# Kernel tuning notes

Hardware: AMD Instinct MI355X
Metric: run time of the kernel (lower is better)

Reference implementation:

```python
import jax, jax.numpy as jnp
import numpy as np

EMBED_DIM = 1024
NUM_HEADS = 16
HEAD_DIM = EMBED_DIM // NUM_HEADS
EPS = 1e-5


def setup_inputs() -> dict:
    key = jax.random.key(0)
    ks = jax.random.split(key, 14)
    B, S, E = 2, 2048, EMBED_DIM
    s = 1.0 / np.sqrt(E)
    inp = {
        "x": jax.random.normal(ks[0], (B, S, E), dtype=jnp.float32),
        "Wq": jax.random.normal(ks[1], (E, E), dtype=jnp.float32) * s,
        "bq": jax.random.normal(ks[2], (E,), dtype=jnp.float32) * 0.01,
        "Wk": jax.random.normal(ks[3], (E, E), dtype=jnp.float32) * s,
        "bk": jax.random.normal(ks[4], (E,), dtype=jnp.float32) * 0.01,
        "Wv": jax.random.normal(ks[5], (E, E), dtype=jnp.float32) * s,
        "bv": jax.random.normal(ks[6], (E,), dtype=jnp.float32) * 0.01,
        "Wo": jax.random.normal(ks[7], (E, E), dtype=jnp.float32) * s,
        "bo": jax.random.normal(ks[8], (E,), dtype=jnp.float32) * 0.01,
        "qn_w": jnp.ones((HEAD_DIM,), jnp.float32) + 0.1 * jax.random.normal(ks[9], (HEAD_DIM,), jnp.float32),
        "qn_b": 0.1 * jax.random.normal(ks[10], (HEAD_DIM,), jnp.float32),
        "kn_w": jnp.ones((HEAD_DIM,), jnp.float32) + 0.1 * jax.random.normal(ks[11], (HEAD_DIM,), jnp.float32),
        "kn_b": 0.1 * jax.random.normal(ks[12], (HEAD_DIM,), jnp.float32),
    }
    return inp


def _layernorm(t, w, b):
    # normalize over last axis (head_dim), matching eqx.nn.LayerNorm(eps=1e-5)
    mu = jnp.mean(t, axis=-1, keepdims=True)
    var = jnp.mean(jnp.square(t - mu), axis=-1, keepdims=True)
    return (t - mu) * jax.lax.rsqrt(var + EPS) * w + b


def reference(x, Wq, bq, Wk, bk, Wv, bv, Wo, bo, qn_w, qn_b, kn_w, kn_b):
    B, S, E = x.shape
    H, D = NUM_HEADS, HEAD_DIM
    q = (x @ Wq.T + bq).reshape(B, S, H, D)
    k = (x @ Wk.T + bk).reshape(B, S, H, D)
    v = (x @ Wv.T + bv).reshape(B, S, H, D)
    q = _layernorm(q, qn_w, qn_b)
    k = _layernorm(k, kn_w, kn_b)
    scale = D ** (-0.5)
    # [B,H,S,S] score matrix (faithful to naive implementation)
    scores = jnp.einsum("bqhd,bkhd->bhqk", q, k) * scale
    attn = jax.nn.softmax(scores, axis=-1)
    out = jnp.einsum("bhqk,bkhd->bqhd", attn, v).reshape(B, S, E)
    return out @ Wo.T + bo
```

## Files before the change

### kernel.cpp

```cpp
#include <hip/hip_runtime.h>
#include <stdint.h>


typedef __bf16 bf16_t;
typedef __bf16 bf16x8 __attribute__((ext_vector_type(8)));
typedef __bf16 bf16x4 __attribute__((ext_vector_type(4)));
typedef __bf16 bf16x2 __attribute__((ext_vector_type(2)));
typedef float f32x4 __attribute__((ext_vector_type(4)));
typedef float f32x16 __attribute__((ext_vector_type(16)));
typedef uint32_t u32x4 __attribute__((ext_vector_type(4)));

#define S_LEN 2048
#define QSCALE 0.1803368801f

__device__ __forceinline__ void load_lds16(const void* g, void* l) {
  __builtin_amdgcn_global_load_lds((__attribute__((address_space(1))) void*)g,
                                   (__attribute__((address_space(3))) void*)l,
                                   16, 0, 0);
}

__device__ __forceinline__ f32x4 mfma16(bf16x8 a, bf16x8 b, f32x4 c) {
  return __builtin_amdgcn_mfma_f32_16x16x32_bf16(a, b, c, 0, 0, 0);
}

__device__ __forceinline__ f32x16 mfma32(bf16x8 a, bf16x8 b, f32x16 c) {
  return __builtin_amdgcn_mfma_f32_32x32x16_bf16(a, b, c, 0, 0, 0);
}

__device__ __forceinline__ uint32_t pk_bf16(float a, float b) {
  bf16x2 v; v[0] = (bf16_t)a; v[1] = (bf16_t)b;
  return __builtin_bit_cast(uint32_t, v);
}

__device__ __forceinline__ void plswap(uint32_t& a, uint32_t& b) {
  asm volatile("v_permlane32_swap_b32 %0, %1" : "+v"(a), "+v"(b));
}

__global__ void cvt_all(const float* __restrict__ x, const float* __restrict__ Wq,
                        const float* __restrict__ Wk, const float* __restrict__ Wv,
                        const float* __restrict__ Wo,
                        bf16_t* __restrict__ xb, bf16_t* __restrict__ Wb,
                        bf16_t* __restrict__ Wob) {
  const int bid = blockIdx.x;
  const float* src; bf16_t* dst; int idx;
  if (bid < 4096) { src = x; dst = xb; idx = bid; }
  else {
    const int r = bid - 4096, rg = r >> 10;
    idx = r & 1023;
    if (rg == 0)      { src = Wq; dst = Wb; }
    else if (rg == 1) { src = Wk; dst = Wb + (1 << 20); }
    else if (rg == 2) { src = Wv; dst = Wb + (2 << 20); }
    else              { src = Wo; dst = Wob; }
  }
  const int i = (idx * 256 + threadIdx.x) * 4;
  float4 v = *reinterpret_cast<const float4*>(src + i);
  bf16x4 o;
  o[0] = (bf16_t)v.x; o[1] = (bf16_t)v.y; o[2] = (bf16_t)v.z; o[3] = (bf16_t)v.w;
  *reinterpret_cast<bf16x4*>(dst + i) = o;
}

__device__ __forceinline__ void gemm_main(const bf16_t* __restrict__ ga,
                                          const bf16_t* __restrict__ gb,
                                          bf16_t* As, bf16_t* Bs,
                                          int t, int wr, int wc, int lg, int lr,
                                          f32x4 (&acc)[4][4]) {
  for (int k0 = 0; k0 < 1024; k0 += 32) {
    load_lds16(ga + k0,          As + t * 8);
    load_lds16(ga + 65536 + k0,  As + 2048 + t * 8);
    load_lds16(gb + k0,          Bs + t * 8);
    load_lds16(gb + 65536 + k0,  Bs + 2048 + t * 8);
    __syncthreads();
    bf16x8 af[4], bfr[4];
#pragma unroll
    for (int mt = 0; mt < 4; ++mt)
      af[mt] = *reinterpret_cast<const bf16x8*>(As + ((wr * 64 + mt * 16 + lr) << 5) + lg * 8);
#pragma unroll
    for (int nt = 0; nt < 4; ++nt)
      bfr[nt] = *reinterpret_cast<const bf16x8*>(Bs + ((wc * 64 + nt * 16 + lr) << 5) + lg * 8);
#pragma unroll
    for (int mt = 0; mt < 4; ++mt)
#pragma unroll
      for (int nt = 0; nt < 4; ++nt)
        acc[mt][nt] = mfma16(af[mt], bfr[nt], acc[mt][nt]);
    __syncthreads();
  }
}

__launch_bounds__(256, 2)
__global__ void gemm_qkv_ln(const bf16_t* __restrict__ A, const bf16_t* __restrict__ Bt,
                            const float* __restrict__ bq, const float* __restrict__ bk,
                            const float* __restrict__ bv,
                            const float* __restrict__ qnw, const float* __restrict__ qnb,
                            const float* __restrict__ knw, const float* __restrict__ knb,
                            bf16_t* __restrict__ Qb, bf16_t* __restrict__ Kb,
                            bf16_t* __restrict__ Vt) {
  __shared__ alignas(16) bf16_t As[128 * 32];
  __shared__ alignas(16) bf16_t Bs[128 * 32];
  const int t = threadIdx.x;
  const int orig = blockIdx.y * 24 + blockIdx.x;
  const int logical = (orig & 7) * 96 + (orig >> 3);
  const int bn = logical % 24, bm = logical / 24;
  const int w = t >> 6, lane = t & 63;
  const int wr = w >> 1, wc = w & 1;
  const int lg = lane >> 4, lr = lane & 15;

  f32x4 acc[4][4] = {};
  const int srow = t >> 2;
  const int scol = (t & 3) << 3;
  const bf16_t* ga = A + ((size_t)(bm * 128 + srow) << 10) + scol;
  const bf16_t* gb = Bt + ((size_t)(bn * 128 + srow) << 10) + scol;
  gemm_main(ga, gb, As, Bs, t, wr, wc, lg, lr, acc);

  const int nbase = bn * 128 + wc * 64;
  const int region = nbase >> 10;
  const int h = (nbase & 1023) >> 6;

  if (region == 2) {
#pragma unroll
    for (int mt = 0; mt < 4; ++mt)
#pragma unroll
      for (int r = 0; r < 4; ++r) {
        const int gm = bm * 128 + wr * 64 + mt * 16 + lg * 4 + r;
        const int b = gm >> 11, s = gm & 2047;
#pragma unroll
        for (int nt = 0; nt < 4; ++nt) {
          const int d = nt * 16 + lr;
          float val = acc[mt][nt][r] + bv[h * 64 + d];
          Vt[((size_t)((b * 16 + h) * 64 + d) << 11) + s] = (bf16_t)val;
        }
      }
  } else {
    const float* bias = region ? bk : bq;
    const float* lw = region ? knw : qnw;
    const float* lb = region ? knb : qnb;
    const float osc = region ? 1.0f : QSCALE;
    bf16_t* Outp = region ? Kb : Qb;
#pragma unroll
    for (int mt = 0; mt < 4; ++mt)
#pragma unroll
      for (int r = 0; r < 4; ++r) {
        const int gm = bm * 128 + wr * 64 + mt * 16 + lg * 4 + r;
        const int b = gm >> 11, s = gm & 2047;
        float vv[4], sum = 0.f, sumsq = 0.f;
#pragma unroll
        for (int nt = 0; nt < 4; ++nt) {
          const int d = nt * 16 + lr;
          vv[nt] = acc[mt][nt][r] + bias[h * 64 + d];
          sum += vv[nt];
          sumsq += vv[nt] * vv[nt];
        }
#pragma unroll
        for (int mk = 1; mk < 16; mk <<= 1) {
          sum += __shfl_xor(sum, mk);
          sumsq += __shfl_xor(sumsq, mk);
        }
        const float mean = sum * (1.f / 64.f);
        const float var = sumsq * (1.f / 64.f) - mean * mean;
        const float rstd = rsqrtf(var + 1e-5f);
        const size_t rowoff = ((size_t)((b * 16 + h) * 2048 + s)) << 6;
#pragma unroll
        for (int nt = 0; nt < 4; ++nt) {
          const int d = nt * 16 + lr;
          float y = ((vv[nt] - mean) * rstd * lw[d] + lb[d]) * osc;
          Outp[rowoff + d] = (bf16_t)y;
        }
      }
  }
}

__launch_bounds__(256, 2)
__global__ void gemm_out(const bf16_t* __restrict__ A, const bf16_t* __restrict__ Bt,
                         const float* __restrict__ bo, float* __restrict__ dout) {
  __shared__ alignas(16) bf16_t As[64 * 32];
  __shared__ alignas(16) bf16_t Bs[128 * 32];
  const int t = threadIdx.x;
  const int orig = blockIdx.y * 8 + blockIdx.x;
  const int logical = (orig & 7) * 64 + (orig >> 3);
  const int bn = logical & 7, bm = logical >> 3;
  const int w = t >> 6, lane = t & 63;
  const int wr = w >> 1, wc = w & 1;
  const int lg = lane >> 4, lr = lane & 15;

  f32x4 acc[2][4] = {};
  const int srow = t >> 2;
  const int scol = (t & 3) << 3;
  const bf16_t* ga = A + ((size_t)(bm * 64 + srow) << 10) + scol;
  const bf16_t* gb = Bt + ((size_t)(bn * 128 + srow) << 10) + scol;

  for (int k0 = 0; k0 < 1024; k0 += 32) {
    load_lds16(ga + k0,          As + t * 8);
    load_lds16(gb + k0,          Bs + t * 8);
    load_lds16(gb + 65536 + k0,  Bs + 2048 + t * 8);
    __syncthreads();
    bf16x8 af[2], bfr[4];
#pragma unroll
    for (int mt = 0; mt < 2; ++mt)
      af[mt] = *reinterpret_cast<const bf16x8*>(As + ((wr * 32 + mt * 16 + lr) << 5) + lg * 8);
#pragma unroll
    for (int nt = 0; nt < 4; ++nt)
      bfr[nt] = *reinterpret_cast<const bf16x8*>(Bs + ((wc * 64 + nt * 16 + lr) << 5) + lg * 8);
#pragma unroll
    for (int mt = 0; mt < 2; ++mt)
#pragma unroll
      for (int nt = 0; nt < 4; ++nt)
        acc[mt][nt] = mfma16(af[mt], bfr[nt], acc[mt][nt]);
    __syncthreads();
  }

#pragma unroll
  for (int mt = 0; mt < 2; ++mt)
#pragma unroll
    for (int r = 0; r < 4; ++r) {
      const int gm = bm * 64 + wr * 32 + mt * 16 + lg * 4 + r;
#pragma unroll
      for (int nt = 0; nt < 4; ++nt) {
        const int gn = bn * 128 + wc * 64 + nt * 16 + lr;
        dout[((size_t)gm << 10) + gn] = acc[mt][nt][r] + bo[gn];
      }
    }
}

template <int NSPLIT>
__launch_bounds__(256, 4)
__global__ void attn_kernel(const bf16_t* __restrict__ Qb, const bf16_t* __restrict__ Kb,
                            const bf16_t* __restrict__ Vt, bf16_t* __restrict__ Og,
                            float* __restrict__ Op, float* __restrict__ Lp) {
  __shared__ alignas(16) bf16_t KVs[4][64 * 64];

  const int t = threadIdx.x;
  const int w = t >> 6, lane = t & 63;
  const int lq = lane & 31;
  const int hi = lane >> 5;
  const int orig = (blockIdx.z * 32 + blockIdx.y) * 16 + blockIdx.x;
  const int logical = (orig & 7) * (64 * NSPLIT) + (orig >> 3);
  const int qt = logical & 15;
  const int bh = (logical >> 4) & 31;
  const int z = (NSPLIT == 1) ? 0 : (logical >> 9);
  const int b = bh >> 4, h = bh & 15;
  const int q0 = qt * 128 + w * 32;
  const int ntiles = 32 / NSPLIT;

  bf16x8 qf[4];
  {
    const bf16_t* qp = Qb + (((size_t)bh * S_LEN + q0 + lq) << 6) + hi * 8;
#pragma unroll
    for (int c = 0; c < 4; ++c)
      qf[c] = *reinterpret_cast<const bf16x8*>(qp + c * 16);
  }

  f32x16 oacc0 = {}, oacc1 = {}, lacc = {};

  const int krow = (t >> 1) & 63;
  const int kch = ((t >> 7) << 1) | (t & 1);
  const bf16_t* kbase = Kb + (((size_t)bh * S_LEN) << 6) + krow * 64 + kch * 8;
  const bf16_t* vbase = Vt + ((size_t)bh << 17) + krow * S_LEN + kch * 8;

#define STAGE(buf, jt)                                                       \
  {                                                                          \
    const bf16_t* kb_ = kbase + (((size_t)(jt)) << 12);                      \
    const bf16_t* vb_ = vbase + (jt) * 64;                                   \
    load_lds16(kb_,      &KVs[buf][t * 8]);                                  \
    load_lds16(kb_ + 32, &KVs[buf][2048 + t * 8]);                           \
    load_lds16(vb_,      &KVs[2 + (buf)][t * 8]);                            \
    load_lds16(vb_ + 32, &KVs[2 + (buf)][2048 + t * 8]);                     \
  }

  STAGE(0, z * ntiles);
  __syncthreads();

  for (int j = 0; j < ntiles; ++j) {
    const int cur = j & 1;
    if (j < ntiles - 1) STAGE(cur ^ 1, z * ntiles + j + 1);

    f32x16 s0 = {}, s1 = {};
    const bf16_t* kr = &KVs[cur][lq * 16 + hi * 8];
#pragma unroll
    for (int c = 0; c < 4; ++c) {
      bf16x8 kf = *reinterpret_cast<const bf16x8*>(kr + c * 1024);
      s0 = mfma32(kf, qf[c], s0);
    }
#pragma unroll
    for (int c = 0; c < 4; ++c) {
      bf16x8 kf = *reinterpret_cast<const bf16x8*>(kr + 512 + c * 1024);
      s1 = mfma32(kf, qf[c], s1);
    }

    f32x16 p0, p1;
#pragma unroll
    for (int i = 0; i < 16; ++i) p0[i] = __builtin_amdgcn_exp2f(s0[i]);
#pragma unroll
    for (int i = 0; i < 16; ++i) p1[i] = __builtin_amdgcn_exp2f(s1[i]);
    lacc += p0;
    lacc += p1;

    const bf16_t* vr = &KVs[2 + cur][lq * 16 + hi * 8];
#pragma unroll
    for (int c = 0; c < 4; ++c) {
      const f32x16 ph = (c < 2) ? p0 : p1;
      const int cl = c & 1;
      uint32_t w00 = pk_bf16(ph[8 * cl + 0], ph[8 * cl + 1]);
      uint32_t w01 = pk_bf16(ph[8 * cl + 2], ph[8 * cl + 3]);
      uint32_t w10 = pk_bf16(ph[8 * cl + 4], ph[8 * cl + 5]);
      uint32_t w11 = pk_bf16(ph[8 * cl + 6], ph[8 * cl + 7]);
      plswap(w00, w10);
      plswap(w01, w11);
      u32x4 pw = {w00, w01, w10, w11};
      bf16x8 pf = __builtin_bit_cast(bf16x8, pw);
      {
        bf16x8 vf = *reinterpret_cast<const bf16x8*>(vr + c * 1024);
        oacc0 = mfma32(vf, pf, oacc0);
      }
      {
        bf16x8 vf = *reinterpret_cast<const bf16x8*>(vr + 512 + c * 1024);
        oacc1 = mfma32(vf, pf, oacc1);
      }
    }
    __syncthreads();
  }

  float l_;
  {
    float sv[8];
#pragma unroll
    for (int i = 0; i < 8; ++i) sv[i] = lacc[i] + lacc[i + 8];
#pragma unroll
    for (int s2 = 4; s2 >= 1; s2 >>= 1)
#pragma unroll
      for (int i = 0; i < s2; ++i) sv[i] += sv[i + s2];
    l_ = sv[0] + __shfl_xor(sv[0], 32);
  }

  if constexpr (NSPLIT == 1) {
    bf16_t* Os = &KVs[0][0] + w * 2048;
    const float inv = __builtin_amdgcn_rcpf(l_);
#pragma unroll
    for (int dh = 0; dh < 2; ++dh) {
      const f32x16 oa = dh ? oacc1 : oacc0;
#pragma unroll
      for (int g = 0; g < 8; ++g) {
        const int reg = g * 2;
        const int dl = (reg & 3) + 8 * (reg >> 2) + 4 * hi;
        const int d = dh * 32 + dl;
        const uint32_t wv = pk_bf16(oa[reg] * inv, oa[reg + 1] * inv);
        const int byte = lq * 128 + ((((d >> 3) ^ (lq & 7))) << 4) + ((d & 7) << 1);
        *reinterpret_cast<uint32_t*>(reinterpret_cast<char*>(Os) + byte) = wv;
      }
    }
#pragma unroll
    for (int it = 0; it < 4; ++it) {
      const int q = it * 8 + (lane >> 3);
      const int ch = lane & 7;
      bf16x8 ov = *reinterpret_cast<const bf16x8*>(
          reinterpret_cast<char*>(Os) + q * 128 + ((ch ^ (q & 7)) << 4));
      const size_t gaddr = (((size_t)(b * S_LEN + q0 + q)) << 10) + h * 64 + ch * 8;
      *reinterpret_cast<bf16x8*>(Og + gaddr) = ov;
    }
  } else {
    float* Os32 = reinterpret_cast<float*>(&KVs[0][0]) + w * 2048;
#pragma unroll
    for (int dh = 0; dh < 2; ++dh) {
      const f32x16 oa = dh ? oacc1 : oacc0;
#pragma unroll
      for (int reg = 0; reg < 16; ++reg) {
        const int dl = (reg & 3) + 8 * (reg >> 2) + 4 * hi;
        const int d = dh * 32 + dl;
        Os32[lq * 64 + (((d >> 2) ^ (lq & 15)) << 2) + (d & 3)] = oa[reg];
      }
    }
    if (lane < 32) Lp[(size_t)(z * 32 + bh) * 2048 + q0 + lq] = l_;
#pragma unroll
    for (int it = 0; it < 4; ++it) {
      const int q = it * 8 + (lane >> 3);
      const size_t rowoff = ((size_t)((z * 32 + bh) * 2048 + q0 + q)) << 6;
#pragma unroll
      for (int c2 = 0; c2 < 2; ++c2) {
        const int ch = ((lane & 7) << 1) + c2;
        f32x4 v = *reinterpret_cast<const f32x4*>(Os32 + q * 64 + ((ch ^ (q & 15)) << 2));
        *reinterpret_cast<f32x4*>(Op + rowoff + (ch << 2)) = v;
      }
    }
  }
#undef STAGE
}

__global__ void attn_combine(const float* __restrict__ Op, const float* __restrict__ Lp,
                             bf16_t* __restrict__ Ob) {
  const int gid = blockIdx.x * 256 + threadIdx.x;
  const int row = gid >> 4, ch = gid & 15;
  const float* o1 = Op + ((size_t)row << 6) + ch * 4;
  const float* o2 = o1 + (1u << 22);
  const float inv = 1.f / (Lp[row] + Lp[(1u << 16) + row]);
  f32x4 v1 = *reinterpret_cast<const f32x4*>(o1);
  f32x4 v2 = *reinterpret_cast<const f32x4*>(o2);
  bf16x4 o;
#pragma unroll
  for (int i = 0; i < 4; ++i) o[i] = (bf16_t)((v1[i] + v2[i]) * inv);
  const int bh = row >> 11, s = row & 2047;
  const int b = bh >> 4, h = bh & 15;
  *reinterpret_cast<bf16x4*>(Ob + (((size_t)(b * S_LEN + s)) << 10) + h * 64 + ch * 4) = o;
}

extern "C" void kernel_launch(void* const* d_in, const int* in_sizes, int n_in,
                              void* d_out, int out_size, void* d_ws, size_t ws_size,
                              hipStream_t stream) {
  const float* x = (const float*)d_in[0];
  const float* Wq = (const float*)d_in[1];
  const float* bq = (const float*)d_in[2];
  const float* Wk = (const float*)d_in[3];
  const float* bk = (const float*)d_in[4];
  const float* Wv = (const float*)d_in[5];
  const float* bv = (const float*)d_in[6];
  const float* Wo = (const float*)d_in[7];
  const float* bo = (const float*)d_in[8];
  const float* qnw = (const float*)d_in[9];
  const float* qnb = (const float*)d_in[10];
  const float* knw = (const float*)d_in[11];
  const float* knb = (const float*)d_in[12];
  float* out = (float*)d_out;

  uint8_t* ws = (uint8_t*)d_ws;
  bf16_t* xb = (bf16_t*)(ws + 0);
  bf16_t* Wb = (bf16_t*)(ws + 8388608);
  bf16_t* Wob = (bf16_t*)(ws + 14680064);
  bf16_t* Qb = (bf16_t*)(ws + 16777216);
  bf16_t* Kb = (bf16_t*)(ws + 25165824);
  bf16_t* Vt = (bf16_t*)(ws + 33554432);
  bf16_t* Ob = (bf16_t*)(ws + 41943040);
  float*  Opart = (float*)(ws + 50331648);
  float*  Lpart = (float*)(ws + 83886080);
  const bool split = ws_size >= 84934656ull;

  cvt_all<<<8192, 256, 0, stream>>>(x, Wq, Wk, Wv, Wo, xb, Wb, Wob);

  gemm_qkv_ln<<<dim3(24, 32), 256, 0, stream>>>(xb, Wb, bq, bk, bv, qnw, qnb, knw, knb,
                                                Qb, Kb, Vt);
  if (split) {
    attn_kernel<2><<<dim3(16, 32, 2), 256, 0, stream>>>(Qb, Kb, Vt, Ob, Opart, Lpart);
    attn_combine<<<4096, 256, 0, stream>>>(Opart, Lpart, Ob);
  } else {
    attn_kernel<1><<<dim3(16, 32, 1), 256, 0, stream>>>(Qb, Kb, Vt, Ob, Opart, Lpart);
  }
  gemm_out<<<dim3(8, 64), 256, 0, stream>>>(Ob, Wob, bo, out);
}
```

Baseline: 122.3 us.

## Double-buffer GEMM LDS tiles and store split-attention partials in bf16

Both GEMM kernels now use two LDS buffers so that the global-to-LDS loads for the next K slice are issued before the MFMAs on the current slice, with one barrier per iteration. This targets load latency that the old load-sync-compute-sync loop exposed. The split-K attention path now writes unnormalized partial outputs in bf16 through the same swizzled LDS staging as the non-split path, and the combine kernel reads them as bf16. This halves partial-buffer traffic at some cost in precision for the unnormalized accumulators, and doubles LDS use in the GEMMs, which could affect occupancy.

After: 117.7 us. -3.7%, faster.

```diff
diff --git a/kernel.cpp b/kernel.cpp
--- a/kernel.cpp
+++ b/kernel.cpp
@@ -59,33 +59,6 @@
   *reinterpret_cast<bf16x4*>(dst + i) = o;
 }
 
-__device__ __forceinline__ void gemm_main(const bf16_t* __restrict__ ga,
-                                          const bf16_t* __restrict__ gb,
-                                          bf16_t* As, bf16_t* Bs,
-                                          int t, int wr, int wc, int lg, int lr,
-                                          f32x4 (&acc)[4][4]) {
-  for (int k0 = 0; k0 < 1024; k0 += 32) {
-    load_lds16(ga + k0,          As + t * 8);
-    load_lds16(ga + 65536 + k0,  As + 2048 + t * 8);
-    load_lds16(gb + k0,          Bs + t * 8);
-    load_lds16(gb + 65536 + k0,  Bs + 2048 + t * 8);
-    __syncthreads();
-    bf16x8 af[4], bfr[4];
-#pragma unroll
-    for (int mt = 0; mt < 4; ++mt)
-      af[mt] = *reinterpret_cast<const bf16x8*>(As + ((wr * 64 + mt * 16 + lr) << 5) + lg * 8);
-#pragma unroll
-    for (int nt = 0; nt < 4; ++nt)
-      bfr[nt] = *reinterpret_cast<const bf16x8*>(Bs + ((wc * 64 + nt * 16 + lr) << 5) + lg * 8);
-#pragma unroll
-    for (int mt = 0; mt < 4; ++mt)
-#pragma unroll
-      for (int nt = 0; nt < 4; ++nt)
-        acc[mt][nt] = mfma16(af[mt], bfr[nt], acc[mt][nt]);
-    __syncthreads();
-  }
-}
-
 __launch_bounds__(256, 2)
 __global__ void gemm_qkv_ln(const bf16_t* __restrict__ A, const bf16_t* __restrict__ Bt,
                             const float* __restrict__ bq, const float* __restrict__ bk,
@@ -94,8 +67,8 @@
                             const float* __restrict__ knw, const float* __restrict__ knb,
                             bf16_t* __restrict__ Qb, bf16_t* __restrict__ Kb,
                             bf16_t* __restrict__ Vt) {
-  __shared__ alignas(16) bf16_t As[128 * 32];
-  __shared__ alignas(16) bf16_t Bs[128 * 32];
+  __shared__ alignas(16) bf16_t As[2][128 * 32];
+  __shared__ alignas(16) bf16_t Bs[2][128 * 32];
   const int t = threadIdx.x;
   const int orig = blockIdx.y * 24 + blockIdx.x;
   const int logical = (orig & 7) * 96 + (orig >> 3);
@@ -109,7 +82,35 @@
   const int scol = (t & 3) << 3;
   const bf16_t* ga = A + ((size_t)(bm * 128 + srow) << 10) + scol;
   const bf16_t* gb = Bt + ((size_t)(bn * 128 + srow) << 10) + scol;
-  gemm_main(ga, gb, As, Bs, t, wr, wc, lg, lr, acc);
+
+#define GSTAGE(buf, k0)                                        \
+  {                                                            \
+    load_lds16(ga + (k0),         &As[buf][t * 8]);            \
+    load_lds16(ga + 65536 + (k0), &As[buf][2048 + t * 8]);     \
+    load_lds16(gb + (k0),         &Bs[buf][t * 8]);            \
+    load_lds16(gb + 65536 + (k0), &Bs[buf][2048 + t * 8]);     \
+  }
+
+  GSTAGE(0, 0);
+  __syncthreads();
+  for (int it = 0; it < 32; ++it) {
+    const int cur = it & 1;
+    if (it < 31) GSTAGE(cur ^ 1, (it + 1) << 5);
+    bf16x8 af[4], bfr[4];
+#pragma unroll
+    for (int mt = 0; mt < 4; ++mt)
+      af[mt] = *reinterpret_cast<const bf16x8*>(&As[cur][((wr * 64 + mt * 16 + lr) << 5) + lg * 8]);
+#pragma unroll
+    for (int nt = 0; nt < 4; ++nt)
+      bfr[nt] = *reinterpret_cast<const bf16x8*>(&Bs[cur][((wc * 64 + nt * 16 + lr) << 5) + lg * 8]);
+#pragma unroll
+    for (int mt = 0; mt < 4; ++mt)
+#pragma unroll
+      for (int nt = 0; nt < 4; ++nt)
+        acc[mt][nt] = mfma16(af[mt], bfr[nt], acc[mt][nt]);
+    __syncthreads();
+  }
+#undef GSTAGE
 
   const int nbase = bn * 128 + wc * 64;
   const int region = nbase >> 10;
@@ -171,8 +172,8 @@
 __launch_bounds__(256, 2)
 __global__ void gemm_out(const bf16_t* __restrict__ A, const bf16_t* __restrict__ Bt,
                          const float* __restrict__ bo, float* __restrict__ dout) {
-  __shared__ alignas(16) bf16_t As[64 * 32];
-  __shared__ alignas(16) bf16_t Bs[128 * 32];
+  __shared__ alignas(16) bf16_t As[2][64 * 32];
+  __shared__ alignas(16) bf16_t Bs[2][128 * 32];
   const int t = threadIdx.x;
   const int orig = blockIdx.y * 8 + blockIdx.x;
   const int logical = (orig & 7) * 64 + (orig >> 3);
@@ -187,18 +188,25 @@
   const bf16_t* ga = A + ((size_t)(bm * 64 + srow) << 10) + scol;
   const bf16_t* gb = Bt + ((size_t)(bn * 128 + srow) << 10) + scol;
 
-  for (int k0 = 0; k0 < 1024; k0 += 32) {
-    load_lds16(ga + k0,          As + t * 8);
-    load_lds16(gb + k0,          Bs + t * 8);
-    load_lds16(gb + 65536 + k0,  Bs + 2048 + t * 8);
-    __syncthreads();
+#define OSTAGE(buf, k0)                                        \
+  {                                                            \
+    load_lds16(ga + (k0),         &As[buf][t * 8]);            \
+    load_lds16(gb + (k0),         &Bs[buf][t * 8]);            \
+    load_lds16(gb + 65536 + (k0), &Bs[buf][2048 + t * 8]);     \
+  }
+
+  OSTAGE(0, 0);
+  __syncthreads();
+  for (int it = 0; it < 32; ++it) {
+    const int cur = it & 1;
+    if (it < 31) OSTAGE(cur ^ 1, (it + 1) << 5);
     bf16x8 af[2], bfr[4];
 #pragma unroll
     for (int mt = 0; mt < 2; ++mt)
-      af[mt] = *reinterpret_cast<const bf16x8*>(As + ((wr * 32 + mt * 16 + lr) << 5) + lg * 8);
+      af[mt] = *reinterpret_cast<const bf16x8*>(&As[cur][((wr * 32 + mt * 16 + lr) << 5) + lg * 8]);
 #pragma unroll
     for (int nt = 0; nt < 4; ++nt)
-      bfr[nt] = *reinterpret_cast<const bf16x8*>(Bs + ((wc * 64 + nt * 16 + lr) << 5) + lg * 8);
+      bfr[nt] = *reinterpret_cast<const bf16x8*>(&Bs[cur][((wc * 64 + nt * 16 + lr) << 5) + lg * 8]);
 #pragma unroll
     for (int mt = 0; mt < 2; ++mt)
 #pragma unroll
@@ -206,6 +214,7 @@
         acc[mt][nt] = mfma16(af[mt], bfr[nt], acc[mt][nt]);
     __syncthreads();
   }
+#undef OSTAGE
 
 #pragma unroll
   for (int mt = 0; mt < 2; ++mt)
@@ -224,7 +233,7 @@
 __launch_bounds__(256, 4)
 __global__ void attn_kernel(const bf16_t* __restrict__ Qb, const bf16_t* __restrict__ Kb,
                             const bf16_t* __restrict__ Vt, bf16_t* __restrict__ Og,
-                            float* __restrict__ Op, float* __restrict__ Lp) {
+                            bf16_t* __restrict__ Op, float* __restrict__ Lp) {
   __shared__ alignas(16) bf16_t KVs[4][64 * 64];
 
   const int t = threadIdx.x;
@@ -330,9 +339,9 @@
     l_ = sv[0] + __shfl_xor(sv[0], 32);
   }
 
-  if constexpr (NSPLIT == 1) {
+  {
     bf16_t* Os = &KVs[0][0] + w * 2048;
-    const float inv = __builtin_amdgcn_rcpf(l_);
+    const float inv = (NSPLIT == 1) ? __builtin_amdgcn_rcpf(l_) : 1.0f;
 #pragma unroll
     for (int dh = 0; dh < 2; ++dh) {
       const f32x16 oa = dh ? oacc1 : oacc0;
@@ -346,58 +355,41 @@
         *reinterpret_cast<uint32_t*>(reinterpret_cast<char*>(Os) + byte) = wv;
       }
     }
+    if (NSPLIT == 2 && lane < 32)
+      Lp[(size_t)(z * 32 + bh) * 2048 + q0 + lq] = l_;
 #pragma unroll
     for (int it = 0; it < 4; ++it) {
       const int q = it * 8 + (lane >> 3);
       const int ch = lane & 7;
       bf16x8 ov = *reinterpret_cast<const bf16x8*>(
           reinterpret_cast<char*>(Os) + q * 128 + ((ch ^ (q & 7)) << 4));
-      const size_t gaddr = (((size_t)(b * S_LEN + q0 + q)) << 10) + h * 64 + ch * 8;
-      *reinterpret_cast<bf16x8*>(Og + gaddr) = ov;
-    }
-  } else {
-    float* Os32 = reinterpret_cast<float*>(&KVs[0][0]) + w * 2048;
-#pragma unroll
-    for (int dh = 0; dh < 2; ++dh) {
-      const f32x16 oa = dh ? oacc1 : oacc0;
-#pragma unroll
-      for (int reg = 0; reg < 16; ++reg) {
-        const int dl = (reg & 3) + 8 * (reg >> 2) + 4 * hi;
-        const int d = dh * 32 + dl;
-        Os32[lq * 64 + (((d >> 2) ^ (lq & 15)) << 2) + (d & 3)] = oa[reg];
-      }
-    }
-    if (lane < 32) Lp[(size_t)(z * 32 + bh) * 2048 + q0 + lq] = l_;
-#pragma unroll
-    for (int it = 0; it < 4; ++it) {
-      const int q = it * 8 + (lane >> 3);
-      const size_t rowoff = ((size_t)((z * 32 + bh) * 2048 + q0 + q)) << 6;
-#pragma unroll
-      for (int c2 = 0; c2 < 2; ++c2) {
-        const int ch = ((lane & 7) << 1) + c2;
-        f32x4 v = *reinterpret_cast<const f32x4*>(Os32 + q * 64 + ((ch ^ (q & 15)) << 2));
-        *reinterpret_cast<f32x4*>(Op + rowoff + (ch << 2)) = v;
+      if constexpr (NSPLIT == 1) {
+        const size_t gaddr = (((size_t)(b * S_LEN + q0 + q)) << 10) + h * 64 + ch * 8;
+        *reinterpret_cast<bf16x8*>(Og + gaddr) = ov;
+      } else {
+        const size_t rowoff = ((size_t)((z * 32 + bh) * 2048 + q0 + q)) << 6;
+        *reinterpret_cast<bf16x8*>(Op + rowoff + ch * 8) = ov;
       }
     }
   }
 #undef STAGE
 }
 
-__global__ void attn_combine(const float* __restrict__ Op, const float* __restrict__ Lp,
+__global__ void attn_combine(const bf16_t* __restrict__ Op, const float* __restrict__ Lp,
                              bf16_t* __restrict__ Ob) {
   const int gid = blockIdx.x * 256 + threadIdx.x;
-  const int row = gid >> 4, ch = gid & 15;
-  const float* o1 = Op + ((size_t)row << 6) + ch * 4;
-  const float* o2 = o1 + (1u << 22);
+  const int row = gid >> 3, ch = gid & 7;
+  const bf16_t* o1 = Op + ((size_t)row << 6) + ch * 8;
+  const bf16_t* o2 = o1 + (1u << 22);
   const float inv = 1.f / (Lp[row] + Lp[(1u << 16) + row]);
-  f32x4 v1 = *reinterpret_cast<const f32x4*>(o1);
-  f32x4 v2 = *reinterpret_cast<const f32x4*>(o2);
-  bf16x4 o;
-#pragma unroll
-  for (int i = 0; i < 4; ++i) o[i] = (bf16_t)((v1[i] + v2[i]) * inv);
+  bf16x8 v1 = *reinterpret_cast<const bf16x8*>(o1);
+  bf16x8 v2 = *reinterpret_cast<const bf16x8*>(o2);
+  bf16x8 o;
+#pragma unroll
+  for (int i = 0; i < 8; ++i) o[i] = (bf16_t)(((float)v1[i] + (float)v2[i]) * inv);
   const int bh = row >> 11, s = row & 2047;
   const int b = bh >> 4, h = bh & 15;
-  *reinterpret_cast<bf16x4*>(Ob + (((size_t)(b * S_LEN + s)) << 10) + h * 64 + ch * 4) = o;
+  *reinterpret_cast<bf16x8*>(Ob + (((size_t)(b * S_LEN + s)) << 10) + h * 64 + ch * 8) = o;
 }
 
 extern "C" void kernel_launch(void* const* d_in, const int* in_sizes, int n_in,
@@ -426,9 +418,9 @@
   bf16_t* Kb = (bf16_t*)(ws + 25165824);
   bf16_t* Vt = (bf16_t*)(ws + 33554432);
   bf16_t* Ob = (bf16_t*)(ws + 41943040);
-  float*  Opart = (float*)(ws + 50331648);
-  float*  Lpart = (float*)(ws + 83886080);
-  const bool split = ws_size >= 84934656ull;
+  bf16_t* Opart = (bf16_t*)(ws + 50331648);
+  float*  Lpart = (float*)(ws + 67108864);
+  const bool split = ws_size >= 67633152ull;
 
   cvt_all<<<8192, 256, 0, stream>>>(x, Wq, Wk, Wv, Wo, xb, Wb, Wob);
 
@@ -436,7 +428,7 @@
                                                 Qb, Kb, Vt);
   if (split) {
     attn_kernel<2><<<dim3(16, 32, 2), 256, 0, stream>>>(Qb, Kb, Vt, Ob, Opart, Lpart);
-    attn_combine<<<4096, 256, 0, stream>>>(Opart, Lpart, Ob);
+    attn_combine<<<2048, 256, 0, stream>>>(Opart, Lpart, Ob);
   } else {
     attn_kernel<1><<<dim3(16, 32, 1), 256, 0, stream>>>(Qb, Kb, Vt, Ob, Opart, Lpart);
   }
```
